# Performance work log

Measured on AMD Instinct MI355X. Metric: run time of the kernel, lower is better.

Reference implementation:

```python
import jax, jax.numpy as jnp
import numpy as np

NEG = -1e30  # finite stand-in for log(0), safe in fp32
EPS = 1e-7   # keras.backend.epsilon()


def ctc_loss(y_true, log_probs):
    """CTC negative log-likelihood, blank = C-1, full label lengths (as in
    keras.backend.ctc_batch_cost with label_length = L, input_length = T).
    y_true: (B, L) int labels in [0, C-1). log_probs: (B, T, C).
    Returns (B, 1) loss, matching ctc_batch_cost's output shape."""
    B, T, C = log_probs.shape
    L = y_true.shape[1]
    S = 2 * L + 1
    blank = C - 1

    # Extended label sequence: blank, l1, blank, l2, ..., lL, blank
    ext = jnp.full((B, S), blank, dtype=y_true.dtype).at[:, 1::2].set(y_true)
    # s-2 skip transition allowed iff ext[s] != blank and ext[s] != ext[s-2]
    skip = jnp.concatenate(
        [jnp.zeros((B, 2), dtype=bool),
         (ext[:, 2:] != blank) & (ext[:, 2:] != ext[:, :-2])], axis=1)

    # Gather per-frame log-probs of extended labels: (B, T, S) -> (T, B, S)
    lp = jnp.take_along_axis(
        log_probs, jnp.broadcast_to(ext[:, None, :], (B, T, S)), axis=2)
    lp = jnp.transpose(lp, (1, 0, 2))

    alpha0 = (jnp.full((B, S), NEG, dtype=log_probs.dtype)
              .at[:, 0].set(lp[0, :, 0])
              .at[:, 1].set(lp[0, :, 1]))
    neg_col = jnp.full((B, 1), NEG, dtype=log_probs.dtype)

    def step(alpha, lp_t):
        a1 = alpha                                            # stay
        a2 = jnp.concatenate([neg_col, alpha[:, :-1]], 1)     # from s-1
        a3 = jnp.where(skip,
                       jnp.concatenate([neg_col, neg_col, alpha[:, :-2]], 1),
                       NEG)                                   # from s-2
        m = jnp.maximum(a1, jnp.maximum(a2, a3))
        new = m + jnp.log(jnp.exp(a1 - m) + jnp.exp(a2 - m) + jnp.exp(a3 - m)) + lp_t
        return new, None

    alphaT, _ = jax.lax.scan(step, alpha0, lp[1:])
    # P(labels | probs) = alpha_T[S-1] + alpha_T[S-2]
    loss = -jnp.logaddexp(alphaT[:, S - 1], alphaT[:, S - 2])
    return loss[:, None]


def setup_inputs() -> dict:
    key = jax.random.key(0)
    k1, k2 = jax.random.split(key)
    B, T, C, L = 512, 512, 256, 128
    # ctc_batch_cost expects probabilities (softmax outputs)
    y_pred = jax.nn.softmax(jax.random.normal(k1, (B, T, C), dtype=jnp.float32), axis=-1)
    y_true = jax.random.randint(k2, (B, L), 0, C - 1, dtype=jnp.int64 if jax.config.jax_enable_x64 else jnp.int32)
    return {"y_true": y_true, "y_pred": y_pred}


def reference(y_true, y_pred):
    log_probs = jnp.log(y_pred + EPS)
    return ctc_loss(y_true, log_probs)
```

## Files before the change

kernel.cpp:

```cpp
#include <hip/hip_runtime.h>

#define NEGF -1e30f
#define EPSF 1e-7f

__global__ __launch_bounds__(256)
void ctc_fwd_kernel(const int* __restrict__ y_true,
                    const float* __restrict__ y_pred,
                    float* __restrict__ out,
                    int T, int C, int L) {
    const int b   = blockIdx.x;
    const int tid = threadIdx.x;

    __shared__ float row[4][256];
    __shared__ float alpha[2][264];

    const float* Yb = y_pred + (size_t)b * T * C;
    const int*   lb = y_true + (size_t)b * L;

    const bool odd = (tid & 1) != 0;
    const int  lab = odd ? lb[tid >> 1] : (C - 1);
    const bool skip = odd && (tid >= 3) && (lab != lb[(tid >> 1) - 1]);

    if (tid < 2) { alpha[0][tid] = NEGF; alpha[1][tid] = NEGF; }

    float r0 = Yb[tid];
    float p0 = Yb[(size_t)1 * C + tid];
    float p1 = Yb[(size_t)2 * C + tid];
    float p2 = Yb[(size_t)3 * C + tid];
    row[0][tid] = r0;
    __syncthreads();

    float a_self;
    if (tid == 0)      a_self = log2f(row[0][C - 1] + EPSF);
    else if (tid == 1) a_self = log2f(row[0][lab]   + EPSF);
    else               a_self = NEGF;
    float a_self2 = NEGF;
    alpha[0][tid + 2] = a_self;

    for (int t = 1; t < T; ++t) {
        const int rb = t & 3;
        row[rb][tid] = p0;
        p0 = p1; p1 = p2;
        if (t + 3 < T) p2 = Yb[(size_t)(t + 3) * C + tid];
        __syncthreads();

        const float* ap = alpha[(t - 1) & 1];
        const float lp = log2f(row[rb][lab] + EPSF);
        const float a1 = a_self;
        const float a2 = ap[tid + 1];
        const float a3 = skip ? ap[tid] : NEGF;
        const float m  = fmaxf(a1, fmaxf(a2, a3));
        const float sum = exp2f(a1 - m) + exp2f(a2 - m) + exp2f(a3 - m);
        const float anew = m + log2f(sum) + lp;
        alpha[t & 1][tid + 2] = anew;

        if (tid == 255) {
            const float lpb = log2f(row[rb][C - 1] + EPSF);
            const float b1 = a_self2;
            const float b2 = a_self;
            const float mb = fmaxf(b1, b2);
            a_self2 = mb + log2f(exp2f(b1 - mb) + exp2f(b2 - mb)) + lpb;
        }
        a_self = anew;
    }

    if (tid == 255) {
        const float x = a_self2, y = a_self;
        const float m = fmaxf(x, y);
        out[b] = -0.69314718055994530942f *
                 (m + log2f(exp2f(x - m) + exp2f(y - m)));
    }
}

extern "C" void kernel_launch(void* const* d_in, const int* in_sizes, int n_in,
                              void* d_out, int out_size, void* d_ws, size_t ws_size,
                              hipStream_t stream) {
    const int*   y_true = (const int*)d_in[0];
    const float* y_pred = (const float*)d_in[1];
    float*       out    = (float*)d_out;

    const int B = out_size;
    const int L = in_sizes[0] / B;
    const int C = 256;
    const int T = in_sizes[1] / (B * C);

    ctc_fwd_kernel<<<B, 256, 0, stream>>>(y_true, y_pred, out, T, C, L);
}
```

Baseline: 540.6 us.

## Run CTC recursion in a single wavefront with register alphas and shuffles

Replaces the 256-thread block, which kept alpha in shared memory and hit a block barrier every time step, with one 64-lane wavefront per sequence. Each lane holds four extended-label states (plus a fifth on the last lane) in registers and takes the left neighbour through __shfl_up, so no __syncthreads is needed. Per-frame probabilities for the lane's labels are gathered straight from global memory and prefetched eight frames ahead in a register ring, with the time loop unrolled by eight. The trade-off is more serial work per lane, five log-sum-exps per step, and lower occupancy per block, in exchange for dropping barriers and LDS traffic.

```diff
diff --git a/kernel.cpp b/kernel.cpp
--- a/kernel.cpp
+++ b/kernel.cpp
@@ -2,73 +2,94 @@
 
 #define NEGF -1e30f
 #define EPSF 1e-7f
+#define LN2F 0.69314718055994530942f
 
-__global__ __launch_bounds__(256)
-void ctc_fwd_kernel(const int* __restrict__ y_true,
-                    const float* __restrict__ y_pred,
-                    float* __restrict__ out,
-                    int T, int C, int L) {
-    const int b   = blockIdx.x;
-    const int tid = threadIdx.x;
+__device__ __forceinline__ float lse2(float x, float y) {
+    float m = fmaxf(x, y);
+    return m + log2f(exp2f(x - m) + exp2f(y - m));
+}
+__device__ __forceinline__ float lse3(float x, float y, float z) {
+    float m = fmaxf(fmaxf(x, y), z);
+    return m + log2f(exp2f(x - m) + exp2f(y - m) + exp2f(z - m));
+}
 
-    __shared__ float row[4][256];
-    __shared__ float alpha[2][264];
-
+__global__ __launch_bounds__(64)
+void ctc_fwd_wave(const int* __restrict__ y_true,
+                  const float* __restrict__ y_pred,
+                  float* __restrict__ out,
+                  int T, int C, int L) {
+    const int b = blockIdx.x;
+    const int l = threadIdx.x;
     const float* Yb = y_pred + (size_t)b * T * C;
     const int*   lb = y_true + (size_t)b * L;
 
-    const bool odd = (tid & 1) != 0;
-    const int  lab = odd ? lb[tid >> 1] : (C - 1);
-    const bool skip = odd && (tid >= 3) && (lab != lb[(tid >> 1) - 1]);
+    const int lab0 = lb[2 * l];
+    const int lab1 = lb[2 * l + 1];
+    const int labP = __shfl_up(lab1, 1);
+    const bool sk1 = (l > 0) && (lab0 != labP);
+    const bool sk3 = (lab1 != lab0);
+    const int cb = C - 1;
 
-    if (tid < 2) { alpha[0][tid] = NEGF; alpha[1][tid] = NEGF; }
-
-    float r0 = Yb[tid];
-    float p0 = Yb[(size_t)1 * C + tid];
-    float p1 = Yb[(size_t)2 * C + tid];
-    float p2 = Yb[(size_t)3 * C + tid];
-    row[0][tid] = r0;
-    __syncthreads();
-
-    float a_self;
-    if (tid == 0)      a_self = log2f(row[0][C - 1] + EPSF);
-    else if (tid == 1) a_self = log2f(row[0][lab]   + EPSF);
-    else               a_self = NEGF;
-    float a_self2 = NEGF;
-    alpha[0][tid + 2] = a_self;
-
-    for (int t = 1; t < T; ++t) {
-        const int rb = t & 3;
-        row[rb][tid] = p0;
-        p0 = p1; p1 = p2;
-        if (t + 3 < T) p2 = Yb[(size_t)(t + 3) * C + tid];
-        __syncthreads();
-
-        const float* ap = alpha[(t - 1) & 1];
-        const float lp = log2f(row[rb][lab] + EPSF);
-        const float a1 = a_self;
-        const float a2 = ap[tid + 1];
-        const float a3 = skip ? ap[tid] : NEGF;
-        const float m  = fmaxf(a1, fmaxf(a2, a3));
-        const float sum = exp2f(a1 - m) + exp2f(a2 - m) + exp2f(a3 - m);
-        const float anew = m + log2f(sum) + lp;
-        alpha[t & 1][tid + 2] = anew;
-
-        if (tid == 255) {
-            const float lpb = log2f(row[rb][C - 1] + EPSF);
-            const float b1 = a_self2;
-            const float b2 = a_self;
-            const float mb = fmaxf(b1, b2);
-            a_self2 = mb + log2f(exp2f(b1 - mb) + exp2f(b2 - mb)) + lpb;
-        }
-        a_self = anew;
+    float a0, a1, a2 = NEGF, a3 = NEGF, a4 = NEGF;
+    {
+        const float pb = Yb[cb];
+        const float p0 = Yb[lab0];
+        a0 = (l == 0) ? log2f(pb + EPSF) : NEGF;
+        a1 = (l == 0) ? log2f(p0 + EPSF) : NEGF;
     }
 
-    if (tid == 255) {
-        const float x = a_self2, y = a_self;
-        const float m = fmaxf(x, y);
-        out[b] = -0.69314718055994530942f *
-                 (m + log2f(exp2f(x - m) + exp2f(y - m)));
+    float rb_[8], r0_[8], r1_[8];
+#pragma unroll
+    for (int k = 1; k <= 8; ++k) {
+        const int s = k & 7;
+        if (k < T) {
+            const float* rp = Yb + (size_t)k * C;
+            rb_[s] = rp[cb];
+            r0_[s] = rp[lab0];
+            r1_[s] = rp[lab1];
+        }
+    }
+
+#define CTC_STEP(S, TCUR)                                                   \
+    do {                                                                    \
+        float pm1 = __shfl_up(a3, 1);       \
+        if (l == 0) pm1 = NEGF;                                             \
+        const float lpb = log2f(rb_[S] + EPSF);                             \
+        const float lp0 = log2f(r0_[S] + EPSF);                             \
+        const float lp1 = log2f(r1_[S] + EPSF);                             \
+        if ((TCUR) + 8 < T) {                      \
+            const float* rp = Yb + (size_t)((TCUR) + 8) * C;                \
+            rb_[S] = rp[cb];                                                \
+            r0_[S] = rp[lab0];                                              \
+            r1_[S] = rp[lab1];                                              \
+        }                                                                   \
+        const float n0 = lse2(a0, pm1) + lpb;                               \
+        const float n1 = lse3(a1, a0, sk1 ? pm1 : NEGF) + lp0;              \
+        const float n2 = lse2(a2, a1) + lpb;                                \
+        const float n3 = lse3(a3, a2, sk3 ? a1 : NEGF) + lp1;               \
+        const float n4 = lse2(a4, a3) + lpb;        \
+        a0 = n0; a1 = n1; a2 = n2; a3 = n3; a4 = n4;                        \
+    } while (0)
+
+    int tb = 1;
+    for (; tb + 8 <= T; tb += 8) {
+#pragma unroll
+        for (int i = 0; i < 8; ++i) {
+            const int s = (1 + i) & 7;
+            CTC_STEP(s, tb + i);
+        }
+    }
+#pragma unroll
+    for (int i = 0; i < 7; ++i) {
+        const int s = (1 + i) & 7;
+        if (tb + i < T) {
+            CTC_STEP(s, tb + i);
+        }
+    }
+#undef CTC_STEP
+
+    if (l == 63) {
+        out[b] = -LN2F * lse2(a4, a3);
     }
 }
 
@@ -84,5 +105,5 @@
     const int C = 256;
     const int T = in_sizes[1] / (B * C);
 
-    ctc_fwd_kernel<<<B, 256, 0, stream>>>(y_true, y_pred, out, T, C, L);
+    ctc_fwd_wave<<<B, 64, 0, stream>>>(y_true, y_pred, out, T, C, L);
 }
```

Result: slower. 698.7 us (+29.3%).

## Split CTC into concurrent forward and backward wavefronts with DPP shifts

Applied to the files above, without the earlier changes.

Replaces the single 256-thread serial alpha recursion with a forward-backward split. One wavefront runs alpha over the first half of the frames and another runs beta over the second half, and the two are combined by a logsumexp reduction at the midpoint. This halves the length of the serial dependency chain. Each lane holds 5 extended-label states in registers and passes neighbours with DPP row shifts instead of shared memory plus __syncthreads. Rows are prefetched through a deep global_load_lds ring with manual vmcnt waits. The costs are more transcendental math per lane, reliance on hard-coded C=256 and L=128, and fragile waitcnt and shift assumptions.

```diff
diff --git a/kernel.cpp b/kernel.cpp
--- a/kernel.cpp
+++ b/kernel.cpp
@@ -2,73 +2,152 @@
 
 #define NEGF -1e30f
 #define EPSF 1e-7f
+#define LN2F 0.69314718055994530942f
+#define DPRE 16
 
-__global__ __launch_bounds__(256)
-void ctc_fwd_kernel(const int* __restrict__ y_true,
-                    const float* __restrict__ y_pred,
-                    float* __restrict__ out,
-                    int T, int C, int L) {
+__device__ __forceinline__ float lse2(float x, float y) {
+    float m = fmaxf(x, y);
+    return m + log2f(exp2f(x - m) + exp2f(y - m));
+}
+__device__ __forceinline__ float lse3(float x, float y, float z) {
+    float m = fmaxf(fmaxf(x, y), z);
+    return m + log2f(exp2f(x - m) + exp2f(y - m) + exp2f(z - m));
+}
+
+__device__ __forceinline__ float wshr1(float v, float fill) {
+    return __int_as_float(__builtin_amdgcn_update_dpp(
+        __float_as_int(fill), __float_as_int(v), 0x138, 0xf, 0xf, false));
+}
+__device__ __forceinline__ float wshl1(float v, float fill) {
+    return __int_as_float(__builtin_amdgcn_update_dpp(
+        __float_as_int(fill), __float_as_int(v), 0x130, 0xf, 0xf, false));
+}
+
+typedef const __attribute__((address_space(1))) void* gptr_t;
+typedef __attribute__((address_space(3))) void* lptr_t;
+__device__ __forceinline__ void gload_row(const float* src, float* dst) {
+    __builtin_amdgcn_global_load_lds((gptr_t)src, (lptr_t)dst, 16, 0, 0);
+}
+
+__global__ __launch_bounds__(128)
+void ctc_fb(const int* __restrict__ y_true,
+            const float* __restrict__ y_pred,
+            float* __restrict__ out,
+            int T, int L) {
+    const int C = 256, cb = 255;
     const int b   = blockIdx.x;
     const int tid = threadIdx.x;
+    const int w   = tid >> 6;
+    const int l   = tid & 63;
+    const int kf  = T >> 1;
 
-    __shared__ float row[4][256];
-    __shared__ float alpha[2][264];
+    __shared__ float buf[2][DPRE][256];
+    __shared__ float comb[260];
 
     const float* Yb = y_pred + (size_t)b * T * C;
     const int*   lb = y_true + (size_t)b * L;
 
-    const bool odd = (tid & 1) != 0;
-    const int  lab = odd ? lb[tid >> 1] : (C - 1);
-    const bool skip = odd && (tid >= 3) && (lab != lb[(tid >> 1) - 1]);
+    const int  lab0 = lb[2 * l];
+    const int  lab1 = lb[2 * l + 1];
+    const int  labP = __shfl_up(lab1, 1);
+    const bool sk1  = (l > 0) && (lab0 != labP);
+    const bool sk3  = (lab1 != lab0);
+    const bool skD  = (l < 63) && (__shfl_down(sk1 ? 1 : 0, 1) != 0);
 
-    if (tid < 2) { alpha[0][tid] = NEGF; alpha[1][tid] = NEGF; }
+    float r0 = NEGF, r1 = NEGF, r2 = NEGF, r3 = NEGF, r4 = NEGF;
 
-    float r0 = Yb[tid];
-    float p0 = Yb[(size_t)1 * C + tid];
-    float p1 = Yb[(size_t)2 * C + tid];
-    float p2 = Yb[(size_t)3 * C + tid];
-    row[0][tid] = r0;
+    if (w == 0) {
+        for (int k = 0; k < DPRE; ++k)
+            gload_row(Yb + (size_t)k * C + 4 * l, &buf[0][k][0]);
+        asm volatile("s_waitcnt vmcnt(15)" ::: "memory");
+        float vb = buf[0][0][cb];
+        float v0 = buf[0][0][lab0];
+        r0 = (l == 0) ? log2f(vb + EPSF) : NEGF;
+        r1 = (l == 0) ? log2f(v0 + EPSF) : NEGF;
+        asm volatile("s_waitcnt vmcnt(14)" ::: "memory");
+        vb = buf[0][1][cb]; v0 = buf[0][1][lab0];
+        float v1 = buf[0][1][lab1];
+
+        for (int i = 0; i < kf; ++i) {
+            const float lpb = log2f(vb + EPSF);
+            const float lp0 = log2f(v0 + EPSF);
+            const float lp1 = log2f(v1 + EPSF);
+            const int fn = DPRE + i;
+            if (fn <= kf)
+                gload_row(Yb + (size_t)fn * C + 4 * l, &buf[0][fn & (DPRE - 1)][0]);
+            asm volatile("s_waitcnt vmcnt(14)" ::: "memory");
+            const int sl = (i + 2) & (DPRE - 1);
+            const float nvb = buf[0][sl][cb];
+            const float nv0 = buf[0][sl][lab0];
+            const float nv1 = buf[0][sl][lab1];
+
+            const float pm1 = wshr1(r3, NEGF);
+            const float n0 = lse2(r0, pm1) + lpb;
+            const float n1 = lse3(r1, r0, sk1 ? pm1 : NEGF) + lp0;
+            const float n2 = lse2(r2, r1) + lpb;
+            const float n3 = lse3(r3, r2, sk3 ? r1 : NEGF) + lp1;
+            const float n4 = lse2(r4, r3) + lpb;
+            r0 = n0; r1 = n1; r2 = n2; r3 = n3; r4 = n4;
+            vb = nvb; v0 = nv0; v1 = nv1;
+        }
+        *(float4*)&comb[4 * l] = make_float4(r0, r1, r2, r3);
+        if (l == 63) comb[256] = r4;
+    } else {
+        for (int k = 0; k < DPRE; ++k) {
+            const int f = T - 1 - k;
+            gload_row(Yb + (size_t)f * C + 4 * l, &buf[1][f & (DPRE - 1)][0]);
+        }
+        r3 = (l == 63) ? 0.0f : NEGF;
+        r4 = (l == 63) ? 0.0f : NEGF;
+        asm volatile("s_waitcnt vmcnt(15)" ::: "memory");
+        const int s0i = (T - 1) & (DPRE - 1);
+        float vb = buf[1][s0i][cb];
+        float v0 = buf[1][s0i][lab0];
+        float v1 = buf[1][s0i][lab1];
+
+        const int NB = T - 1 - kf;
+        for (int j = 0; j < NB; ++j) {
+            const float lpb = log2f(vb + EPSF);
+            const float lp0 = log2f(v0 + EPSF);
+            const float lp1 = log2f(v1 + EPSF);
+            const int fn = T - 1 - (DPRE + j);
+            if (fn > kf)
+                gload_row(Yb + (size_t)fn * C + 4 * l, &buf[1][fn & (DPRE - 1)][0]);
+            asm volatile("s_waitcnt vmcnt(15)" ::: "memory");
+            const int sl = (T - 2 - j) & (DPRE - 1);
+            const float nvb = buf[1][sl][cb];
+            const float nv0 = buf[1][sl][lab0];
+            const float nv1 = buf[1][sl][lab1];
+
+            const float c0 = r0 + lpb;
+            const float c1 = r1 + lp0;
+            const float c2 = r2 + lpb;
+            const float c3 = r3 + lp1;
+            const float c4 = r4 + lpb;
+            float d0 = wshl1(c0, NEGF);
+            const float d1 = wshl1(c1, NEGF);
+            if (l == 63) d0 = c4;
+            const float n0 = lse2(c0, c1);
+            const float n1 = lse3(c1, c2, sk3 ? c3 : NEGF);
+            const float n2 = lse2(c2, c3);
+            const float n3 = lse3(c3, d0, skD ? d1 : NEGF);
+            r0 = n0; r1 = n1; r2 = n2; r3 = n3; r4 = c4;
+            vb = nvb; v0 = nv0; v1 = nv1;
+        }
+    }
     __syncthreads();
 
-    float a_self;
-    if (tid == 0)      a_self = log2f(row[0][C - 1] + EPSF);
-    else if (tid == 1) a_self = log2f(row[0][lab]   + EPSF);
-    else               a_self = NEGF;
-    float a_self2 = NEGF;
-    alpha[0][tid + 2] = a_self;
-
-    for (int t = 1; t < T; ++t) {
-        const int rb = t & 3;
-        row[rb][tid] = p0;
-        p0 = p1; p1 = p2;
-        if (t + 3 < T) p2 = Yb[(size_t)(t + 3) * C + tid];
-        __syncthreads();
-
-        const float* ap = alpha[(t - 1) & 1];
-        const float lp = log2f(row[rb][lab] + EPSF);
-        const float a1 = a_self;
-        const float a2 = ap[tid + 1];
-        const float a3 = skip ? ap[tid] : NEGF;
-        const float m  = fmaxf(a1, fmaxf(a2, a3));
-        const float sum = exp2f(a1 - m) + exp2f(a2 - m) + exp2f(a3 - m);
-        const float anew = m + log2f(sum) + lp;
-        alpha[t & 1][tid + 2] = anew;
-
-        if (tid == 255) {
-            const float lpb = log2f(row[rb][C - 1] + EPSF);
-            const float b1 = a_self2;
-            const float b2 = a_self;
-            const float mb = fmaxf(b1, b2);
-            a_self2 = mb + log2f(exp2f(b1 - mb) + exp2f(b2 - mb)) + lpb;
-        }
-        a_self = anew;
-    }
-
-    if (tid == 255) {
-        const float x = a_self2, y = a_self;
-        const float m = fmaxf(x, y);
-        out[b] = -0.69314718055994530942f *
-                 (m + log2f(exp2f(x - m) + exp2f(y - m)));
+    if (w == 1) {
+        const float4 av = *(const float4*)&comb[4 * l];
+        const float s0 = av.x + r0, s1 = av.y + r1;
+        const float s2 = av.z + r2, s3 = av.w + r3;
+        const float s4 = (l == 63) ? (comb[256] + r4) : NEGF;
+        float m = fmaxf(fmaxf(fmaxf(s0, s1), fmaxf(s2, s3)), s4);
+        for (int o = 32; o; o >>= 1) m = fmaxf(m, __shfl_xor(m, o));
+        float p = exp2f(s0 - m) + exp2f(s1 - m) + exp2f(s2 - m)
+                + exp2f(s3 - m) + exp2f(s4 - m);
+        for (int o = 32; o; o >>= 1) p += __shfl_xor(p, o);
+        if (l == 0) out[b] = -LN2F * (m + log2f(p));
     }
 }
 
@@ -84,5 +163,5 @@
     const int C = 256;
     const int T = in_sizes[1] / (B * C);
 
-    ctc_fwd_kernel<<<B, 256, 0, stream>>>(y_true, y_pred, out, T, C, L);
+    ctc_fb<<<B, 128, 0, stream>>>(y_true, y_pred, out, T, L);
 }
```

Result: faster. 433.2 us (-19.9%).
